# Optimization experiments

Measured on AMD Instinct MI355X. Metric: run time of the kernel, lower is better.

## Reference

```python
import jax, jax.numpy as jnp
import numpy as np

B, Hs, Ws, C = 4, 56, 56, 128
NH, K = 4, 7


def _layernorm(x, w, b, eps=1e-5):
    mu = jnp.mean(x, axis=-1, keepdims=True)
    var = jnp.mean((x - mu) ** 2, axis=-1, keepdims=True)
    return (x - mu) * jax.lax.rsqrt(var + eps) * w + b


def setup_inputs() -> dict:
    key = jax.random.key(0)
    ks = jax.random.split(key, 16)
    s = lambda k_, shape, fan: jax.random.normal(k_, shape, jnp.float32) * (fan ** -0.5)
    hid = 4 * C
    return {
        "x": jax.random.normal(ks[0], (B, Hs, Ws, C), jnp.float32),
        "norm1_w": jnp.ones((C,), jnp.float32),
        "norm1_b": jnp.zeros((C,), jnp.float32),
        "qkv_w": s(ks[1], (3 * C, C), C),
        "qkv_b": jnp.zeros((3 * C,), jnp.float32),
        "rpb": 0.02 * jax.random.normal(ks[2], (NH, 2 * K - 1, 2 * K - 1), jnp.float32),
        "proj_w": s(ks[3], (C, C), C),
        "proj_b": jnp.zeros((C,), jnp.float32),
        "norm2_w": jnp.ones((C,), jnp.float32),
        "norm2_b": jnp.zeros((C,), jnp.float32),
        "fc1_w": s(ks[4], (hid, C), C),
        "fc1_b": jnp.zeros((hid,), jnp.float32),
        "fc2_w": s(ks[5], (C, hid), hid),
        "fc2_b": jnp.zeros((C,), jnp.float32),
    }


def _neighborhood_attention(x, qkv_w, qkv_b, rpb, proj_w, proj_b):
    # x: [B, H, W, C]; NATTEN-style clamped sliding-window attention.
    b, h, w, c = x.shape
    nh = rpb.shape[0]
    k = (rpb.shape[1] + 1) // 2
    hd = c // nh
    scale = hd ** -0.5

    # static clamped window start indices (windows shifted to stay in-bounds)
    sh = np.clip(np.arange(h) - k // 2, 0, h - k)
    sw = np.clip(np.arange(w) - k // 2, 0, w - k)
    idx_h = sh[:, None] + np.arange(k)                  # [H, k]
    idx_w = sw[:, None] + np.arange(k)                  # [W, k]
    bias_h = idx_h - np.arange(h)[:, None] + (k - 1)    # [H, k] in [0, 2k-2]
    bias_w = idx_w - np.arange(w)[:, None] + (k - 1)    # [W, k]

    qkv = x @ qkv_w.T + qkv_b                           # [B,H,W,3C]
    qkv = qkv.reshape(b, h, w, 3, nh, hd)
    q = qkv[..., 0, :, :] * scale                       # [B,H,W,nh,hd]
    kk = qkv[..., 1, :, :]
    vv = qkv[..., 2, :, :]

    # gather neighborhood keys/values: [B,H,kh,W,kw,nh,hd]
    k_win = kk[:, idx_h][:, :, :, idx_w]
    v_win = vv[:, idx_h][:, :, :, idx_w]

    # attention scores + relative positional bias
    scores = jnp.einsum('bhwnd,bhiwjnd->bnhwij', q, k_win)   # [B,nh,H,W,kh,kw]
    bias = rpb[:, bias_h][:, :, :, bias_w]                   # [nh,H,kh,W,kw]
    bias = jnp.transpose(bias, (0, 1, 3, 2, 4))              # [nh,H,W,kh,kw]
    scores = scores + bias[None]

    attn = jax.nn.softmax(scores.reshape(b, nh, h, w, k * k), axis=-1)
    attn = attn.reshape(b, nh, h, w, k, k)
    out = jnp.einsum('bnhwij,bhiwjnd->bhwnd', attn, v_win)   # [B,H,W,nh,hd]
    out = out.reshape(b, h, w, c)
    return out @ proj_w.T + proj_b


def reference(x, norm1_w, norm1_b, qkv_w, qkv_b, rpb, proj_w, proj_b,
              norm2_w, norm2_b, fc1_w, fc1_b, fc2_w, fc2_b):
    # attention block (pre-norm, residual)
    y = _layernorm(x, norm1_w, norm1_b)
    y = _neighborhood_attention(y, qkv_w, qkv_b, rpb, proj_w, proj_b)
    x = x + y
    # MLP block
    z = _layernorm(x, norm2_w, norm2_b)
    z = jax.nn.gelu(z @ fc1_w.T + fc1_b, approximate=False)
    z = z @ fc2_w.T + fc2_b
    return x + z
```

## Files before the change

kernel.cpp:

```cpp
#include <hip/hip_runtime.h>
#include <math.h>

#define TOK 12544
#define CDIM 128
#define NHEAD 4
#define HD 32
#define KS 7
#define HSZ 56
#define WSZ 56

typedef __attribute__((ext_vector_type(8))) short short8;
typedef __attribute__((ext_vector_type(4))) float f32x4;

__device__ inline ushort f2b(float f) {
    uint u = __float_as_uint(f);
    u += 0x7fffu + ((u >> 16) & 1u);
    return (ushort)(u >> 16);
}

__global__ void convert_w(const float* __restrict__ a, const float* __restrict__ b,
                          const float* __restrict__ c, const float* __restrict__ d,
                          ushort* __restrict__ wb) {
    int e = (blockIdx.x * 256 + threadIdx.x) * 4;
    const float* src;
    if (e < 49152)       src = a + e;
    else if (e < 65536)  src = b + (e - 49152);
    else if (e < 131072) src = c + (e - 65536);
    else                 src = d + (e - 131072);
    float4 v = *(const float4*)src;
    uint2 pk;
    pk.x = (uint)f2b(v.x) | ((uint)f2b(v.y) << 16);
    pk.y = (uint)f2b(v.z) | ((uint)f2b(v.w) << 16);
    *(uint2*)(wb + e) = pk;
}

__device__ inline void ln_to_lds(const float* __restrict__ X, int m0,
                                 const float* __restrict__ lnw, const float* __restrict__ lnb,
                                 ushort* __restrict__ lds) {
    int wv = threadIdx.x >> 6, lane = threadIdx.x & 63;
    #pragma unroll
    for (int r = 0; r < 8; r++) {
        int rl = wv * 8 + r;
        float2 v = *(const float2*)(X + (size_t)(m0 + rl) * CDIM + lane * 2);
        float s = v.x + v.y;
        #pragma unroll
        for (int o = 32; o > 0; o >>= 1) s += __shfl_xor(s, o);
        float mu = s * (1.0f / 128.0f);
        float d0 = v.x - mu, d1 = v.y - mu;
        float sq = d0 * d0 + d1 * d1;
        #pragma unroll
        for (int o = 32; o > 0; o >>= 1) sq += __shfl_xor(sq, o);
        float rstd = rsqrtf(sq * (1.0f / 128.0f) + 1e-5f);
        float2 wv2 = *(const float2*)(lnw + lane * 2);
        float2 bv2 = *(const float2*)(lnb + lane * 2);
        uint pk = (uint)f2b(d0 * rstd * wv2.x + bv2.x)
                | ((uint)f2b(d1 * rstd * wv2.y + bv2.y) << 16);
        *(uint*)((char*)lds + rl * 256 + ((lane * 4) ^ ((rl & 7) << 4))) = pk;
    }
}

__global__ __launch_bounds__(512) void ln1_qkv(const float* __restrict__ X,
                                               const ushort* __restrict__ W,
                                               const float* __restrict__ bias,
                                               const float* __restrict__ lnw,
                                               const float* __restrict__ lnb,
                                               ushort* __restrict__ Y) {
    __shared__ ushort xn[64 * 128];
    int m0 = blockIdx.x * 64;
    ln_to_lds(X, m0, lnw, lnb, xn);
    __syncthreads();

    int wv = threadIdx.x >> 6, lane = threadIdx.x & 63;
    int lr = lane & 15, kg = lane >> 4;
    int n0 = wv * 48;
    f32x4 acc[4][3] = {};
    #pragma unroll
    for (int k0 = 0; k0 < 128; k0 += 32) {
        short8 bf[3];
        #pragma unroll
        for (int ni = 0; ni < 3; ni++)
            bf[ni] = *(const short8*)(W + (size_t)(n0 + ni * 16 + lr) * 128 + k0 + kg * 8);
        #pragma unroll
        for (int mg = 0; mg < 4; mg++) {
            int row = mg * 16 + lr;
            short8 a0 = *(const short8*)((char*)xn + row * 256 + ((k0 * 2 + kg * 16) ^ ((row & 7) << 4)));
            #pragma unroll
            for (int ni = 0; ni < 3; ni++)
                acc[mg][ni] = __builtin_amdgcn_mfma_f32_16x16x32_bf16(a0, bf[ni], acc[mg][ni], 0, 0, 0);
        }
    }
    #pragma unroll
    for (int mg = 0; mg < 4; mg++)
    #pragma unroll
    for (int ni = 0; ni < 3; ni++) {
        int base = n0 + ni * 16;
        int which = base >> 7;
        int rem   = base & 127;
        int head  = rem >> 5;
        int hd0   = rem & 31;
        float bn = bias[base + lr];
        float sc = (which == 0) ? 0.17677669529663687f : 1.0f;
        ushort* dst = Y + ((size_t)(which * 4 + head) * TOK) * HD + hd0 + lr;
        #pragma unroll
        for (int r = 0; r < 4; r++) {
            int row = m0 + mg * 16 + kg * 4 + r;
            float v = (acc[mg][ni][r] + bn) * sc;
            dst[(size_t)row * HD] = f2b(v);
        }
    }
}

__global__ __launch_bounds__(512) void proj_mlp(const ushort* __restrict__ aob,
                                                const ushort* __restrict__ Wp,
                                                const float* __restrict__ bp,
                                                const float* __restrict__ X,
                                                const ushort* __restrict__ W1,
                                                const float* __restrict__ b1,
                                                const ushort* __restrict__ W2,
                                                const float* __restrict__ b2,
                                                const float* __restrict__ lnw,
                                                const float* __restrict__ lnb,
                                                float* __restrict__ out) {
    __shared__ float  x2f[64 * 132];
    __shared__ ushort zn[64 * 128];
    __shared__ ushort hb[64 * 256];
    int m0 = blockIdx.x * 64;
    int wv = threadIdx.x >> 6, lane = threadIdx.x & 63;
    int lr = lane & 15, kg = lane >> 4;

    {
        int n0 = wv * 16;
        f32x4 accp[4] = {};
        #pragma unroll
        for (int k0 = 0; k0 < 128; k0 += 32) {
            short8 bf = *(const short8*)(Wp + (size_t)(n0 + lr) * 128 + k0 + kg * 8);
            #pragma unroll
            for (int mg = 0; mg < 4; mg++) {
                short8 a0 = *(const short8*)(aob + (size_t)(m0 + mg * 16 + lr) * 128 + k0 + kg * 8);
                accp[mg] = __builtin_amdgcn_mfma_f32_16x16x32_bf16(a0, bf, accp[mg], 0, 0, 0);
            }
        }
        float bn = bp[n0 + lr];
        #pragma unroll
        for (int mg = 0; mg < 4; mg++)
        #pragma unroll
        for (int r = 0; r < 4; r++) {
            int row = mg * 16 + kg * 4 + r;
            x2f[row * 132 + n0 + lr] = accp[mg][r] + bn
                                     + X[(size_t)(m0 + row) * CDIM + n0 + lr];
        }
    }
    __syncthreads();

    #pragma unroll
    for (int r = 0; r < 8; r++) {
        int rl = wv * 8 + r;
        float2 v = *(const float2*)&x2f[rl * 132 + lane * 2];
        float s = v.x + v.y;
        #pragma unroll
        for (int o = 32; o > 0; o >>= 1) s += __shfl_xor(s, o);
        float mu = s * (1.0f / 128.0f);
        float d0 = v.x - mu, d1 = v.y - mu;
        float sq = d0 * d0 + d1 * d1;
        #pragma unroll
        for (int o = 32; o > 0; o >>= 1) sq += __shfl_xor(sq, o);
        float rstd = rsqrtf(sq * (1.0f / 128.0f) + 1e-5f);
        float2 wv2 = *(const float2*)(lnw + lane * 2);
        float2 bv2 = *(const float2*)(lnb + lane * 2);
        uint pk = (uint)f2b(d0 * rstd * wv2.x + bv2.x)
                | ((uint)f2b(d1 * rstd * wv2.y + bv2.y) << 16);
        *(uint*)((char*)zn + rl * 256 + ((lane * 4) ^ ((rl & 7) << 4))) = pk;
    }

    int rw0 = (wv >> 2) * 32, cw0 = (wv & 3) * 32;
    f32x4 acc2[2][2] = {};
    __syncthreads();

    #pragma unroll
    for (int p = 0; p < 2; p++) {
        f32x4 acc1[4][2] = {};
        int nc0 = wv * 32;
        #pragma unroll
        for (int k0 = 0; k0 < 128; k0 += 32) {
            short8 bf[2];
            #pragma unroll
            for (int ni = 0; ni < 2; ni++)
                bf[ni] = *(const short8*)(W1 + (size_t)(p * 256 + nc0 + ni * 16 + lr) * 128 + k0 + kg * 8);
            #pragma unroll
            for (int mg = 0; mg < 4; mg++) {
                int row = mg * 16 + lr;
                short8 a0 = *(const short8*)((char*)zn + row * 256 + ((k0 * 2 + kg * 16) ^ ((row & 7) << 4)));
                #pragma unroll
                for (int ni = 0; ni < 2; ni++)
                    acc1[mg][ni] = __builtin_amdgcn_mfma_f32_16x16x32_bf16(a0, bf[ni], acc1[mg][ni], 0, 0, 0);
            }
        }
        #pragma unroll
        for (int mg = 0; mg < 4; mg++)
        #pragma unroll
        for (int ni = 0; ni < 2; ni++) {
            int lc = nc0 + ni * 16 + lr;
            float bn = b1[p * 256 + lc];
            #pragma unroll
            for (int r = 0; r < 4; r++) {
                int row = mg * 16 + kg * 4 + r;
                float v = acc1[mg][ni][r] + bn;
                float t = v + 0.044715f * v * v * v;
                float sg = 1.0f / (1.0f + __expf(-1.5957691216f * t));
                v = v * sg;
                *(ushort*)((char*)hb + row * 512 + ((lc * 2) ^ ((row & 7) << 4))) = f2b(v);
            }
        }
        __syncthreads();

        #pragma unroll
        for (int k0 = 0; k0 < 256; k0 += 32) {
            short8 a0[2], bf[2];
            #pragma unroll
            for (int mi = 0; mi < 2; mi++) {
                int row = rw0 + mi * 16 + lr;
                a0[mi] = *(const short8*)((char*)hb + row * 512 + ((k0 * 2 + kg * 16) ^ ((row & 7) << 4)));
            }
            #pragma unroll
            for (int ni = 0; ni < 2; ni++)
                bf[ni] = *(const short8*)(W2 + (size_t)(cw0 + ni * 16 + lr) * 512 + p * 256 + k0 + kg * 8);
            #pragma unroll
            for (int mi = 0; mi < 2; mi++)
            #pragma unroll
            for (int ni = 0; ni < 2; ni++)
                acc2[mi][ni] = __builtin_amdgcn_mfma_f32_16x16x32_bf16(a0[mi], bf[ni], acc2[mi][ni], 0, 0, 0);
        }
        __syncthreads();
    }

    #pragma unroll
    for (int mi = 0; mi < 2; mi++)
    #pragma unroll
    for (int ni = 0; ni < 2; ni++) {
        int col = cw0 + ni * 16 + lr;
        float bn = b2[col];
        #pragma unroll
        for (int r = 0; r < 4; r++) {
            int row = rw0 + mi * 16 + kg * 4 + r;
            out[(size_t)(m0 + row) * CDIM + col] = acc2[mi][ni][r] + bn + x2f[row * 132 + col];
        }
    }
}

__global__ __launch_bounds__(256) void nat_attn7(const ushort* __restrict__ qkv,
                                                 const float* __restrict__ rpb,
                                                 ushort* __restrict__ ao) {
    __shared__ ushort katt[8704];
    __shared__ ushort vs[32 * 232];
    __shared__ float rpl[169];
    ushort* ks = katt;

    int tid = threadIdx.x, wv = tid >> 6, lane = tid & 63;
    int lr = lane & 15, kg = lane >> 4;
    int bid = blockIdx.x;
    int blk = (bid & 7) * 98 + (bid >> 3);
    int tile = blk % 49, hb2 = blk / 49;
    int head = hb2 & 3, b = hb2 >> 2;
    int r0 = (tile / 7) * 8, c0 = (tile % 7) * 8;
    int hr0 = min(max(r0 - 3, 0), HSZ - 14);
    int hc0 = min(max(c0 - 3, 0), WSZ - 14);
    int bimg = b * HSZ * WSZ;

    const ushort* qb = qkv + (size_t)(0 + head) * TOK * HD;
    const ushort* kb = qkv + (size_t)(4 + head) * TOK * HD;
    const ushort* vb = qkv + (size_t)(8 + head) * TOK * HD;

    if (tid < 169) rpl[tid] = rpb[head * 169 + tid];
    for (int idx = tid; idx < 784; idx += 256) {
        int t = idx >> 2, c = idx & 3;
        int gtok = bimg + (hr0 + t / 14) * WSZ + hc0 + t % 14;
        short8 v = *(const short8*)(kb + (size_t)gtok * HD + c * 8);
        *(short8*)(ks + t * 32 + ((c ^ (t & 3)) << 3)) = v;
    }
    for (int idx = tid; idx < 392; idx += 256) {
        int pr = idx >> 2, c = idx & 3;
        int t = pr * 2;
        int gtok = bimg + (hr0 + t / 14) * WSZ + hc0 + t % 14;
        const ushort* vp = vb + (size_t)gtok * HD + c * 8;
        short8 v0 = *(const short8*)vp;
        short8 v1 = *(const short8*)(vp + HD);
        #pragma unroll
        for (int q = 0; q < 8; q++)
            *(uint*)(vs + (c * 8 + q) * 232 + t) =
                (uint)(ushort)v0[q] | ((uint)(ushort)v1[q] << 16);
    }
    for (int idx = tid; idx < 32 * 18; idx += 256)
        *(uint*)(vs + (idx / 18) * 232 + 196 + (idx % 18) * 2) = 0;
    __syncthreads();

    int i0 = r0 + 2 * wv;
    int hw0 = min(max(i0 - 3, 0), HSZ - KS);
    int dwr = hw0 - hr0;
    int tbase = dwr * 14;
    int rb = tbase & ~7;
    int rboff = tbase - rb;

    int lpix = lr;
    int agp = bimg + (r0 + 2 * wv + (lpix >> 3)) * WSZ + c0 + (lpix & 7);
    short8 aq = *(const short8*)(qb + (size_t)agp * HD + kg * 8);
    f32x4 sc[7];
    #pragma unroll
    for (int tl = 0; tl < 7; tl++) {
        int t = tbase + tl * 16 + lr;
        short8 bk = *(const short8*)(ks + t * 32 + ((kg ^ (t & 3)) << 3));
        f32x4 z = {0.f, 0.f, 0.f, 0.f};
        sc[tl] = __builtin_amdgcn_mfma_f32_16x16x32_bf16(aq, bk, z, 0, 0, 0);
    }
    __syncthreads();

    ushort* attw = katt + wv * 16 * 136;
    #pragma unroll
    for (int z = 0; z < 16; z++) {
        int ii = z * 64 + lane;
        *(uint*)(attw + (ii >> 6) * 136 + (ii & 63) * 2) = 0;
    }
    float inv[4];
    #pragma unroll
    for (int r = 0; r < 4; r++) {
        int idx = kg * 4 + r;
        int i = r0 + 2 * wv + (idx >> 3), j = c0 + (idx & 7);
        int shh = min(max(i - 3, 0), HSZ - KS);
        int sww = min(max(j - 3, 0), WSZ - KS);
        int dih = shh - hr0, dj = sww - hc0;
        int offh = hr0 - i + 6, offw = hc0 - j + 6;
        float sv[7];
        float mx = -1e30f;
        #pragma unroll
        for (int tl = 0; tl < 7; tl++) {
            int t = tbase + tl * 16 + lr;
            int thr = (unsigned)t / 14u;
            int twr = t - thr * 14;
            bool in = ((unsigned)(thr - dih) < 7u) && ((unsigned)(twr - dj) < 7u);
            int bidx = (thr + offh) * 13 + (twr + offw);
            bidx = min(max(bidx, 0), 168);
            float s = sc[tl][r] + rpl[bidx];
            sv[tl] = in ? s : -1e30f;
            mx = fmaxf(mx, sv[tl]);
        }
        #pragma unroll
        for (int o = 8; o > 0; o >>= 1) mx = fmaxf(mx, __shfl_xor(mx, o));
        float sum = 0.f;
        #pragma unroll
        for (int tl = 0; tl < 7; tl++) {
            float e = __expf(sv[tl] - mx);
            sum += e;
            attw[idx * 136 + rboff + tl * 16 + lr] = f2b(e);
        }
        #pragma unroll
        for (int o = 8; o > 0; o >>= 1) sum += __shfl_xor(sum, o);
        inv[r] = 1.0f / sum;
    }

    f32x4 po[2] = {};
    #pragma unroll
    for (int kst = 0; kst < 4; kst++) {
        short8 pa = *(const short8*)(attw + lr * 136 + kst * 32 + kg * 8);
        #pragma unroll
        for (int n = 0; n < 2; n++) {
            short8 vbf = *(const short8*)(vs + (n * 16 + lr) * 232 + rb + kst * 32 + kg * 8);
            po[n] = __builtin_amdgcn_mfma_f32_16x16x32_bf16(pa, vbf, po[n], 0, 0, 0);
        }
    }

    #pragma unroll
    for (int n = 0; n < 2; n++)
    #pragma unroll
    for (int rr = 0; rr < 4; rr++) {
        int idx = kg * 4 + rr;
        int gp = bimg + (r0 + 2 * wv + (idx >> 3)) * WSZ + c0 + (idx & 7);
        ao[(size_t)gp * CDIM + head * HD + n * 16 + lr] = f2b(po[n][rr] * inv[rr]);
    }
}

extern "C" void kernel_launch(void* const* d_in, const int* in_sizes, int n_in,
                              void* d_out, int out_size, void* d_ws, size_t ws_size,
                              hipStream_t stream) {
    const float* x      = (const float*)d_in[0];
    const float* n1w    = (const float*)d_in[1];
    const float* n1b    = (const float*)d_in[2];
    const float* qkv_w  = (const float*)d_in[3];
    const float* qkv_b  = (const float*)d_in[4];
    const float* rpb    = (const float*)d_in[5];
    const float* proj_w = (const float*)d_in[6];
    const float* proj_b = (const float*)d_in[7];
    const float* n2w    = (const float*)d_in[8];
    const float* n2b    = (const float*)d_in[9];
    const float* fc1_w  = (const float*)d_in[10];
    const float* fc1_b  = (const float*)d_in[11];
    const float* fc2_w  = (const float*)d_in[12];
    const float* fc2_b  = (const float*)d_in[13];
    float* out = (float*)d_out;

    ushort* wb   = (ushort*)d_ws;
    ushort* qkvb = wb + 196608;
    ushort* aob  = qkvb + (size_t)TOK * 384;

    const ushort* w_qkv  = wb;
    const ushort* w_proj = wb + 49152;
    const ushort* w_fc1  = wb + 65536;
    const ushort* w_fc2  = wb + 131072;

    convert_w<<<192, 256, 0, stream>>>(qkv_w, proj_w, fc1_w, fc2_w, wb);
    ln1_qkv<<<TOK / 64, 512, 0, stream>>>(x, w_qkv, qkv_b, n1w, n1b, qkvb);
    nat_attn7<<<4 * NHEAD * 49, 256, 0, stream>>>(qkvb, rpb, aob);
    proj_mlp<<<TOK / 64, 512, 0, stream>>>(aob, w_proj, proj_b, x,
                                           w_fc1, fc1_b, w_fc2, fc2_b, n2w, n2b, out);
}
```

Baseline: 59.29 us.

## Drop softmax max pass, single-pass layernorm stats, bf16 residual staging in LDS

The neighborhood-attention softmax drops its max-subtraction pass and shuffle reduction, exponentiating scores directly and zeroing only the padding columns outside the valid key range. Both layernorms compute sum and sum-of-squares in one fused shuffle reduction instead of two sequential ones. The proj_mlp kernel stores the residual in LDS as bf16 rather than fp32, shrinking its shared-memory footprint, and adds a launch-bounds occupancy hint. These cut reduction latency, LDS stores and LDS size, but risk overflow without the max shift, cancellation in E[x^2]-mu^2, and lower precision in the residual added to the output.

```diff
diff --git a/kernel.cpp b/kernel.cpp
--- a/kernel.cpp
+++ b/kernel.cpp
@@ -17,6 +17,7 @@
     u += 0x7fffu + ((u >> 16) & 1u);
     return (ushort)(u >> 16);
 }
+__device__ inline float b2f(ushort u) { return __uint_as_float((uint)u << 16); }
 
 __global__ void convert_w(const float* __restrict__ a, const float* __restrict__ b,
                           const float* __restrict__ c, const float* __restrict__ d,
@@ -42,15 +43,17 @@
     for (int r = 0; r < 8; r++) {
         int rl = wv * 8 + r;
         float2 v = *(const float2*)(X + (size_t)(m0 + rl) * CDIM + lane * 2);
-        float s = v.x + v.y;
-        #pragma unroll
-        for (int o = 32; o > 0; o >>= 1) s += __shfl_xor(s, o);
+        float s  = v.x + v.y;
+        float s2 = v.x * v.x + v.y * v.y;
+        #pragma unroll
+        for (int o = 32; o > 0; o >>= 1) {
+            s  += __shfl_xor(s, o);
+            s2 += __shfl_xor(s2, o);
+        }
         float mu = s * (1.0f / 128.0f);
+        float var = s2 * (1.0f / 128.0f) - mu * mu;
+        float rstd = rsqrtf(var + 1e-5f);
         float d0 = v.x - mu, d1 = v.y - mu;
-        float sq = d0 * d0 + d1 * d1;
-        #pragma unroll
-        for (int o = 32; o > 0; o >>= 1) sq += __shfl_xor(sq, o);
-        float rstd = rsqrtf(sq * (1.0f / 128.0f) + 1e-5f);
         float2 wv2 = *(const float2*)(lnw + lane * 2);
         float2 bv2 = *(const float2*)(lnb + lane * 2);
         uint pk = (uint)f2b(d0 * rstd * wv2.x + bv2.x)
@@ -110,18 +113,18 @@
     }
 }
 
-__global__ __launch_bounds__(512) void proj_mlp(const ushort* __restrict__ aob,
-                                                const ushort* __restrict__ Wp,
-                                                const float* __restrict__ bp,
-                                                const float* __restrict__ X,
-                                                const ushort* __restrict__ W1,
-                                                const float* __restrict__ b1,
-                                                const ushort* __restrict__ W2,
-                                                const float* __restrict__ b2,
-                                                const float* __restrict__ lnw,
-                                                const float* __restrict__ lnb,
-                                                float* __restrict__ out) {
-    __shared__ float  x2f[64 * 132];
+__global__ __launch_bounds__(512, 4) void proj_mlp(const ushort* __restrict__ aob,
+                                                   const ushort* __restrict__ Wp,
+                                                   const float* __restrict__ bp,
+                                                   const float* __restrict__ X,
+                                                   const ushort* __restrict__ W1,
+                                                   const float* __restrict__ b1,
+                                                   const ushort* __restrict__ W2,
+                                                   const float* __restrict__ b2,
+                                                   const float* __restrict__ lnw,
+                                                   const float* __restrict__ lnb,
+                                                   float* __restrict__ out) {
+    __shared__ ushort x2b[64 * 132];
     __shared__ ushort zn[64 * 128];
     __shared__ ushort hb[64 * 256];
     int m0 = blockIdx.x * 64;
@@ -146,8 +149,8 @@
         #pragma unroll
         for (int r = 0; r < 4; r++) {
             int row = mg * 16 + kg * 4 + r;
-            x2f[row * 132 + n0 + lr] = accp[mg][r] + bn
-                                     + X[(size_t)(m0 + row) * CDIM + n0 + lr];
+            float v = accp[mg][r] + bn + X[(size_t)(m0 + row) * CDIM + n0 + lr];
+            x2b[row * 132 + n0 + lr] = f2b(v);
         }
     }
     __syncthreads();
@@ -155,16 +158,20 @@
     #pragma unroll
     for (int r = 0; r < 8; r++) {
         int rl = wv * 8 + r;
-        float2 v = *(const float2*)&x2f[rl * 132 + lane * 2];
-        float s = v.x + v.y;
-        #pragma unroll
-        for (int o = 32; o > 0; o >>= 1) s += __shfl_xor(s, o);
+        uint pk2 = *(const uint*)(x2b + rl * 132 + lane * 2);
+        float vx = b2f((ushort)(pk2 & 0xffff));
+        float vy = b2f((ushort)(pk2 >> 16));
+        float s  = vx + vy;
+        float s2 = vx * vx + vy * vy;
+        #pragma unroll
+        for (int o = 32; o > 0; o >>= 1) {
+            s  += __shfl_xor(s, o);
+            s2 += __shfl_xor(s2, o);
+        }
         float mu = s * (1.0f / 128.0f);
-        float d0 = v.x - mu, d1 = v.y - mu;
-        float sq = d0 * d0 + d1 * d1;
-        #pragma unroll
-        for (int o = 32; o > 0; o >>= 1) sq += __shfl_xor(sq, o);
-        float rstd = rsqrtf(sq * (1.0f / 128.0f) + 1e-5f);
+        float var = s2 * (1.0f / 128.0f) - mu * mu;
+        float rstd = rsqrtf(var + 1e-5f);
+        float d0 = vx - mu, d1 = vy - mu;
         float2 wv2 = *(const float2*)(lnw + lane * 2);
         float2 bv2 = *(const float2*)(lnb + lane * 2);
         uint pk = (uint)f2b(d0 * rstd * wv2.x + bv2.x)
@@ -242,12 +249,13 @@
         #pragma unroll
         for (int r = 0; r < 4; r++) {
             int row = rw0 + mi * 16 + kg * 4 + r;
-            out[(size_t)(m0 + row) * CDIM + col] = acc2[mi][ni][r] + bn + x2f[row * 132 + col];
-        }
-    }
-}
-
-__global__ __launch_bounds__(256) void nat_attn7(const ushort* __restrict__ qkv,
+            out[(size_t)(m0 + row) * CDIM + col] = acc2[mi][ni][r] + bn
+                                                 + b2f(x2b[row * 132 + col]);
+        }
+    }
+}
+
+__global__ __launch_bounds__(256) void nat_attn8(const ushort* __restrict__ qkv,
                                                  const float* __restrict__ rpb,
                                                  ushort* __restrict__ ao) {
     __shared__ ushort katt[8704];
@@ -315,10 +323,13 @@
 
     ushort* attw = katt + wv * 16 * 136;
     #pragma unroll
-    for (int z = 0; z < 16; z++) {
+    for (int z = 0; z < 2; z++) {
         int ii = z * 64 + lane;
-        *(uint*)(attw + (ii >> 6) * 136 + (ii & 63) * 2) = 0;
-    }
+        int row = ii >> 3, c2 = (ii & 7) * 2;
+        int col = c2 + (c2 < rboff ? 0 : 112);
+        *(uint*)(attw + row * 136 + col) = 0;
+    }
+
     float inv[4];
     #pragma unroll
     for (int r = 0; r < 4; r++) {
@@ -328,8 +339,7 @@
         int sww = min(max(j - 3, 0), WSZ - KS);
         int dih = shh - hr0, dj = sww - hc0;
         int offh = hr0 - i + 6, offw = hc0 - j + 6;
-        float sv[7];
-        float mx = -1e30f;
+        float sum = 0.f;
         #pragma unroll
         for (int tl = 0; tl < 7; tl++) {
             int t = tbase + tl * 16 + lr;
@@ -338,16 +348,7 @@
             bool in = ((unsigned)(thr - dih) < 7u) && ((unsigned)(twr - dj) < 7u);
             int bidx = (thr + offh) * 13 + (twr + offw);
             bidx = min(max(bidx, 0), 168);
-            float s = sc[tl][r] + rpl[bidx];
-            sv[tl] = in ? s : -1e30f;
-            mx = fmaxf(mx, sv[tl]);
-        }
-        #pragma unroll
-        for (int o = 8; o > 0; o >>= 1) mx = fmaxf(mx, __shfl_xor(mx, o));
-        float sum = 0.f;
-        #pragma unroll
-        for (int tl = 0; tl < 7; tl++) {
-            float e = __expf(sv[tl] - mx);
+            float e = in ? __expf(sc[tl][r] + rpl[bidx]) : 0.f;
             sum += e;
             attw[idx * 136 + rboff + tl * 16 + lr] = f2b(e);
         }
@@ -407,7 +408,7 @@
 
     convert_w<<<192, 256, 0, stream>>>(qkv_w, proj_w, fc1_w, fc2_w, wb);
     ln1_qkv<<<TOK / 64, 512, 0, stream>>>(x, w_qkv, qkv_b, n1w, n1b, qkvb);
-    nat_attn7<<<4 * NHEAD * 49, 256, 0, stream>>>(qkvb, rpb, aob);
+    nat_attn8<<<4 * NHEAD * 49, 256, 0, stream>>>(qkvb, rpb, aob);
     proj_mlp<<<TOK / 64, 512, 0, stream>>>(aob, w_proj, proj_b, x,
                                            w_fc1, fc1_b, w_fc2, fc2_b, n2w, n2b, out);
 }
```

Result: slower. 61.78 us (+4.2%).
